# Optimization experiments

Hardware: AMD Instinct MI355X
Metric: run time of the kernel (lower is better)

Reference implementation:

```python
import jax, jax.numpy as jnp
import numpy as np

WS = (4, 4, 4)          # window size per axis
DISP = (2, 2, 2)        # cyclic-shift displacement = window_size // 2
HEADS = 8
HEAD_DIM = 32
DIM = 256


def _make_mask(x_shift, y_shift, z_shift):
    wx, wy, wz = WS
    dx, dy, dz = DISP
    m = np.zeros((wx, wy, wz, wx, wy, wz), np.float32)
    if x_shift:
        m[-dx:, :, :, :-dx, :, :] = -np.inf
        m[:-dx, :, :, -dx:, :, :] = -np.inf
    if y_shift:
        m[:, -dy:, :, :, :-dy, :] = -np.inf
        m[:, :-dy, :, :, -dy:, :] = -np.inf
    if z_shift:
        m[:, :, -dz:, :, :, :-dz] = -np.inf
        m[:, :, :-dz, :, :, -dz:] = -np.inf
    W = wx * wy * wz
    return jnp.asarray(m.reshape(W, W))


def setup_inputs() -> dict:
    key = jax.random.key(0)
    k1, k2, k3 = jax.random.split(key, 3)
    inner = HEADS * HEAD_DIM
    x = jax.random.normal(k1, (1, 48, 48, 48, DIM), jnp.float32)
    w_qkv = jax.random.normal(k2, (DIM, 3 * inner), jnp.float32) * (DIM ** -0.5)
    w_out = jax.random.normal(k3, (inner, DIM), jnp.float32) * (inner ** -0.5)
    b_out = jnp.zeros((DIM,), jnp.float32)
    return {"x": x, "w_qkv": w_qkv, "w_out": w_out, "b_out": b_out}


def reference(x, w_qkv, w_out, b_out):
    wx, wy, wz = WS
    h, d = HEADS, HEAD_DIM
    scale = d ** -0.5
    xm = _make_mask(True, False, False)
    ym = _make_mask(False, True, False)
    zm = _make_mask(False, False, True)

    # cyclic shift
    x = jnp.roll(x, (-DISP[0], -DISP[1], -DISP[2]), axis=(1, 2, 3))
    b, nx, ny, nz, _ = x.shape
    nwx, nwy, nwz = nx // wx, ny // wy, nz // wz
    W = wx * wy * wz
    nw = nwx * nwy * nwz

    qkv = x @ w_qkv                      # [b,nx,ny,nz,3*h*d]
    q, k, v = jnp.split(qkv, 3, axis=-1)

    def win(t):
        t = t.reshape(b, nwx, wx, nwy, wy, nwz, wz, h, d)
        t = t.transpose(0, 7, 1, 3, 5, 2, 4, 6, 8)   # b h nwx nwy nwz wx wy wz d
        return t.reshape(b, h, nw, W, d)

    q, k, v = win(q), win(k), win(v)
    dots = jnp.einsum('bhwid,bhwjd->bhwij', q, k) * scale

    # additive shift masks on the last window along each axis
    dots = dots.reshape(b, h, nwx, nwy, nwz, W, W)
    dots = dots.at[:, :, -1, :, :].add(xm)
    dots = dots.at[:, :, :, -1, :].add(ym)
    dots = dots.at[:, :, :, :, -1].add(zm)
    # faithful replication of original einops label mismatch: the tensor is
    # (nwx,nwy,nwz) but is flattened as if labeled (n_y,n_z,n_x) -> (n_x n_y n_z),
    # i.e. actual flatten order (nwz, nwx, nwy)
    dots = dots.transpose(0, 1, 4, 2, 3, 5, 6).reshape(b, h, nw, W, W)

    attn = jax.nn.softmax(dots, axis=-1)
    out = jnp.einsum('bhwij,bhwjd->bhwid', attn, v)

    out = out.reshape(b, h, nwx, nwy, nwz, wx, wy, wz, d)
    out = out.transpose(0, 2, 5, 3, 6, 4, 7, 1, 8).reshape(b, nx, ny, nz, h * d)
    out = out @ w_out + b_out
    # cyclic back shift
    return jnp.roll(out, DISP, axis=(1, 2, 3))
```

## Files before the change

kernel.cpp:

```cpp
#include <hip/hip_runtime.h>
#include <hip/hip_bf16.h>

typedef __attribute__((ext_vector_type(8))) short short8;
typedef __attribute__((ext_vector_type(4))) float f32x4;

#define NT 110592

static __device__ __forceinline__ unsigned int f2bf(float f){
  unsigned int x; __builtin_memcpy(&x,&f,4);
  x += 0x7fffu + ((x>>16)&1u);
  return x >> 16;
}

static __device__ __forceinline__ void gll16(const unsigned short* g, unsigned short* l){
  typedef const __attribute__((address_space(1))) unsigned int gu32;
  typedef __attribute__((address_space(3))) unsigned int lu32;
  __builtin_amdgcn_global_load_lds((gu32*)(const void*)g, (lu32*)(void*)l, 16, 0, 0);
}

__global__ void tpose(const float* __restrict__ in, unsigned short* __restrict__ out,
                      int R, int Cc){
  int id = blockIdx.x*256 + threadIdx.x;
  if (id < R*Cc){ int r = id / Cc, c = id - r*Cc; out[c*R + r] = (unsigned short)f2bf(in[id]); }
}

template<bool CF32, bool AF32>
__global__ __launch_bounds__(512, 8) void gemm_bt(
    const void* __restrict__ Av,
    const unsigned short* __restrict__ Bt,
    const float* __restrict__ bias,
    void* __restrict__ Cv,
    int M, int N, int K)
{
  __shared__ __align__(16) unsigned short As[2*4096];
  __shared__ __align__(16) unsigned short Bs[2*4096];

  const int nwg = gridDim.x;
  const int bid = blockIdx.x;
  const int qq = nwg >> 3, rr = nwg & 7;
  const int xcd = bid & 7, loc = bid >> 3;
  const int swz = (xcd < rr ? xcd*(qq+1) : rr*(qq+1) + (xcd-rr)*qq) + loc;
  const int nbn = N >> 7;
  const int bn = swz % nbn;
  const int bm = swz / nbn;

  const int tid  = threadIdx.x;
  const int lane = tid & 63;
  const int wave = tid >> 6;
  const int wm = wave >> 1, wn = wave & 1;
  const int l16 = lane & 15, q = lane >> 4;

  const int g8  = ((tid&3) ^ ((tid>>3)&3)) * 8;
  const int cg8 = (q ^ ((l16>>1)&3)) * 8;

  const size_t arow0 = (size_t)(bm*128 + (tid>>2))*K;
  const size_t brow0 = (size_t)(bn*128 + (tid>>2))*K;
  const unsigned short* Ab = (const unsigned short*)Av;
  const float*          Af = (const float*)Av;

  f32x4 acc[2][4] = {};

  for (int k0 = 0; k0 < K; k0 += 64){
    __syncthreads();
    if (AF32){
      const float* xa0 = Af + arow0 + k0 + g8;
      float4 a0 = *(const float4*)(xa0),      a1 = *(const float4*)(xa0+4);
      float4 b0 = *(const float4*)(xa0+32),   b1 = *(const float4*)(xa0+36);
      gll16(Bt + brow0 + k0 + g8,       &Bs[tid*8]);
      gll16(Bt + brow0 + k0 + 32 + g8,  &Bs[4096 + tid*8]);
      uint4 p0, p1;
      p0.x = f2bf(a0.x)|(f2bf(a0.y)<<16); p0.y = f2bf(a0.z)|(f2bf(a0.w)<<16);
      p0.z = f2bf(a1.x)|(f2bf(a1.y)<<16); p0.w = f2bf(a1.z)|(f2bf(a1.w)<<16);
      p1.x = f2bf(b0.x)|(f2bf(b0.y)<<16); p1.y = f2bf(b0.z)|(f2bf(b0.w)<<16);
      p1.z = f2bf(b1.x)|(f2bf(b1.y)<<16); p1.w = f2bf(b1.z)|(f2bf(b1.w)<<16);
      *(uint4*)&As[tid*8]        = p0;
      *(uint4*)&As[4096 + tid*8] = p1;
    } else {
      gll16(Ab + arow0 + k0 + g8,       &As[tid*8]);
      gll16(Ab + arow0 + k0 + 32 + g8,  &As[4096 + tid*8]);
      gll16(Bt + brow0 + k0 + g8,       &Bs[tid*8]);
      gll16(Bt + brow0 + k0 + 32 + g8,  &Bs[4096 + tid*8]);
    }
    __syncthreads();

    #pragma unroll
    for (int h = 0; h < 2; ++h){
      short8 af[2], bfm[4];
      #pragma unroll
      for (int t = 0; t < 2; ++t)
        af[t]  = *(const short8*)&As[h*4096 + (wm*32 + t*16 + l16)*32 + cg8];
      #pragma unroll
      for (int t = 0; t < 4; ++t)
        bfm[t] = *(const short8*)&Bs[h*4096 + (wn*64 + t*16 + l16)*32 + cg8];
      #pragma unroll
      for (int im = 0; im < 2; ++im)
        #pragma unroll
        for (int in = 0; in < 4; ++in)
          acc[im][in] = __builtin_amdgcn_mfma_f32_16x16x32_bf16(af[im], bfm[in], acc[im][in], 0, 0, 0);
    }
  }

  #pragma unroll
  for (int in = 0; in < 4; ++in){
    int col = bn*128 + wn*64 + in*16 + l16;
    float bv = CF32 ? bias[col] : 0.f;
    #pragma unroll
    for (int im = 0; im < 2; ++im){
      int row0 = bm*128 + wm*32 + im*16 + q*4;
      #pragma unroll
      for (int r = 0; r < 4; ++r){
        if (CF32) ((float*)Cv)[(size_t)(row0 + r)*N + col] = acc[im][in][r] + bv;
        else ((unsigned short*)Cv)[(size_t)(row0 + r)*N + col] = (unsigned short)f2bf(acc[im][in][r]);
      }
    }
  }
}

__global__ __launch_bounds__(256) void attn3d(
    const unsigned short* __restrict__ qkv,
    unsigned short* __restrict__ aout)
{
  __shared__ __align__(16) unsigned short sh[4*6912];
  const int tid  = threadIdx.x;
  const int wave = tid >> 6, lane = tid & 63;
  const int l16  = lane & 15, q = lane >> 4;
  unsigned short* P  = sh + wave*6912;
  unsigned short* VT = P + 64*72;

  const int wh   = blockIdx.x*4 + wave;
  const int head = wh & 7;
  const int w    = wh >> 3;
  const int A  = w / 144;
  const int B  = (w / 12) % 12;
  const int Cw = w % 12;

  const int iyy = l16 >> 2, izz = l16 & 3;
  int tok_qk[4], tok_v[4];
  #pragma unroll
  for (int t = 0; t < 4; ++t){
    int px = (4*B  + t   + 2) % 48;
    int py = (4*Cw + iyy + 2) % 48;
    int pz = (4*A  + izz + 2) % 48;
    tok_qk[t] = (px*48 + py)*48 + pz;
    int vx = (4*A  + t   + 2) % 48;
    int vy = (4*B  + iyy + 2) % 48;
    int vz = (4*Cw + izz + 2) % 48;
    tok_v[t] = (vx*48 + vy)*48 + vz;
  }

  {
    int sx = (4*A  + (lane>>4)     + 2) % 48;
    int sy = (4*B  + ((lane>>2)&3) + 2) % 48;
    int sz = (4*Cw + (lane&3)      + 2) % 48;
    const unsigned short* vp = qkv + (size_t)((sx*48+sy)*48+sz)*768 + 512 + head*32;
    uint4 v0 = *(const uint4*)(vp);
    uint4 v1 = *(const uint4*)(vp+8);
    uint4 v2 = *(const uint4*)(vp+16);
    uint4 v3 = *(const uint4*)(vp+24);
    unsigned vv[16] = {v0.x,v0.y,v0.z,v0.w, v1.x,v1.y,v1.z,v1.w,
                       v2.x,v2.y,v2.z,v2.w, v3.x,v3.y,v3.z,v3.w};
    #pragma unroll
    for (int u = 0; u < 16; ++u){
      VT[(2*u+0)*72 + lane] = (unsigned short)(vv[u] & 0xffffu);
      VT[(2*u+1)*72 + lane] = (unsigned short)(vv[u] >> 16);
    }
  }

  short8 kf[4], qf[4];
  #pragma unroll
  for (int t = 0; t < 4; ++t){
    const unsigned short* base = qkv + (size_t)tok_qk[t]*768 + head*32 + q*8;
    qf[t] = *(const short8*)(base);
    kf[t] = *(const short8*)(base + 256);
  }

  f32x4 s[4][4] = {};
  #pragma unroll
  for (int im = 0; im < 4; ++im)
    #pragma unroll
    for (int jn = 0; jn < 4; ++jn)
      s[im][jn] = __builtin_amdgcn_mfma_f32_16x16x32_bf16(kf[im], qf[jn], s[im][jn], 0, 0, 0);

  const float scale = 0.17677669529663687f;
  const int mx = (B == 11), my = (Cw == 11), mz = (A == 11);
  const int dy = my & ((q>>1) ^ (l16>>3));
  float sum4[4] = {0.f,0.f,0.f,0.f};
  #pragma unroll
  for (int jn = 0; jn < 4; ++jn){
    #pragma unroll
    for (int im = 0; im < 4; ++im){
      const int dxy = (mx & ((im>>1) ^ (jn>>1))) | dy;
      float e0 = (dxy | (mz & (0 ^ ((l16>>1)&1)))) ? 0.f : __expf(s[im][jn][0]*scale);
      float e1 = (dxy | (mz & (0 ^ ((l16>>1)&1)))) ? 0.f : __expf(s[im][jn][1]*scale);
      float e2 = (dxy | (mz & (1 ^ ((l16>>1)&1)))) ? 0.f : __expf(s[im][jn][2]*scale);
      float e3 = (dxy | (mz & (1 ^ ((l16>>1)&1)))) ? 0.f : __expf(s[im][jn][3]*scale);
      sum4[jn] += (e0+e1)+(e2+e3);
      uint2 pk;
      pk.x = f2bf(e0) | (f2bf(e1)<<16);
      pk.y = f2bf(e2) | (f2bf(e3)<<16);
      *(uint2*)&P[(jn*16+l16)*72 + im*16 + q*4] = pk;
    }
  }
  #pragma unroll
  for (int jn = 0; jn < 4; ++jn){
    float sj = sum4[jn];
    sj += __shfl_xor(sj, 16);
    sj += __shfl_xor(sj, 32);
    sum4[jn] = 1.f / sj;
  }

  f32x4 o[2][4] = {};
  #pragma unroll
  for (int ks = 0; ks < 2; ++ks){
    short8 vf[2], pf[4];
    #pragma unroll
    for (int dt = 0; dt < 2; ++dt)
      vf[dt] = *(const short8*)&VT[(dt*16 + l16)*72 + ks*32 + q*8];
    #pragma unroll
    for (int it = 0; it < 4; ++it)
      pf[it] = *(const short8*)&P[(it*16 + l16)*72 + ks*32 + q*8];
    #pragma unroll
    for (int dt = 0; dt < 2; ++dt)
      #pragma unroll
      for (int it = 0; it < 4; ++it)
        o[dt][it] = __builtin_amdgcn_mfma_f32_16x16x32_bf16(vf[dt], pf[it], o[dt][it], 0, 0, 0);
  }

  #pragma unroll
  for (int it = 0; it < 4; ++it){
    float inv = sum4[it];
    unsigned short* op = aout + (size_t)tok_v[it]*256 + head*32;
    #pragma unroll
    for (int dt = 0; dt < 2; ++dt){
      uint2 pk;
      pk.x = f2bf(o[dt][it][0]*inv) | (f2bf(o[dt][it][1]*inv) << 16);
      pk.y = f2bf(o[dt][it][2]*inv) | (f2bf(o[dt][it][3]*inv) << 16);
      *(uint2*)(op + dt*16 + q*4) = pk;
    }
  }
}

extern "C" void kernel_launch(void* const* d_in, const int* in_sizes, int n_in,
                              void* d_out, int out_size, void* d_ws, size_t ws_size,
                              hipStream_t stream) {
  const float* x     = (const float*)d_in[0];
  const float* w_qkv = (const float*)d_in[1];
  const float* w_out = (const float*)d_in[2];
  const float* b_out = (const float*)d_in[3];
  float* out = (float*)d_out;

  unsigned short* qkv   = (unsigned short*)d_ws;
  unsigned short* aout  = qkv   + (size_t)NT*768;
  unsigned short* wqkvT = aout  + (size_t)NT*256;
  unsigned short* woutT = wqkvT + (size_t)768*256;

  tpose<<<dim3((256*768 + 255)/256), dim3(256), 0, stream>>>(w_qkv, wqkvT, 256, 768);
  tpose<<<dim3((256*256 + 255)/256), dim3(256), 0, stream>>>(w_out, woutT, 256, 256);

  gemm_bt<false, true><<<dim3((768/128)*(NT/128)), dim3(512), 0, stream>>>(
      (const void*)x, wqkvT, nullptr, qkv, NT, 768, 256);

  attn3d<<<dim3(13824/4), dim3(256), 0, stream>>>(qkv, aout);

  gemm_bt<true, false><<<dim3((256/128)*(NT/128)), dim3(512), 0, stream>>>(
      (const void*)aout, woutT, b_out, out, NT, 256, 256);
}
```

Measured before the change: 377.0 us.

## Double-buffer GEMM LDS tiles to overlap next-slab loads with MFMA compute

Restructures the GEMM main loop from a single-buffered 64-wide K step into a 32-wide slab loop that ping-pongs between two LDS buffers. The loads for the next slab, including async global-to-LDS copies and the fp32 A loads, are issued before the MFMAs on the current slab, and the bf16 conversion store follows the compute. This cuts one barrier per iteration and hides global load latency behind compute. In exchange there are twice as many loop iterations, each with less MFMA work, and more registers are live.

New measurement: 805.4 us. 2.14x slower.

```diff
diff --git a/kernel.cpp b/kernel.cpp
--- a/kernel.cpp
+++ b/kernel.cpp
@@ -59,44 +59,58 @@
   const float*          Af = (const float*)Av;
 
   f32x4 acc[2][4] = {};
-
-  for (int k0 = 0; k0 < K; k0 += 64){
-    __syncthreads();
-    if (AF32){
-      const float* xa0 = Af + arow0 + k0 + g8;
-      float4 a0 = *(const float4*)(xa0),      a1 = *(const float4*)(xa0+4);
-      float4 b0 = *(const float4*)(xa0+32),   b1 = *(const float4*)(xa0+36);
-      gll16(Bt + brow0 + k0 + g8,       &Bs[tid*8]);
-      gll16(Bt + brow0 + k0 + 32 + g8,  &Bs[4096 + tid*8]);
-      uint4 p0, p1;
-      p0.x = f2bf(a0.x)|(f2bf(a0.y)<<16); p0.y = f2bf(a0.z)|(f2bf(a0.w)<<16);
-      p0.z = f2bf(a1.x)|(f2bf(a1.y)<<16); p0.w = f2bf(a1.z)|(f2bf(a1.w)<<16);
-      p1.x = f2bf(b0.x)|(f2bf(b0.y)<<16); p1.y = f2bf(b0.z)|(f2bf(b0.w)<<16);
-      p1.z = f2bf(b1.x)|(f2bf(b1.y)<<16); p1.w = f2bf(b1.z)|(f2bf(b1.w)<<16);
-      *(uint4*)&As[tid*8]        = p0;
-      *(uint4*)&As[4096 + tid*8] = p1;
-    } else {
-      gll16(Ab + arow0 + k0 + g8,       &As[tid*8]);
-      gll16(Ab + arow0 + k0 + 32 + g8,  &As[4096 + tid*8]);
-      gll16(Bt + brow0 + k0 + g8,       &Bs[tid*8]);
-      gll16(Bt + brow0 + k0 + 32 + g8,  &Bs[4096 + tid*8]);
-    }
-    __syncthreads();
-
-    #pragma unroll
-    for (int h = 0; h < 2; ++h){
-      short8 af[2], bfm[4];
+  const int nslab = K >> 5;
+
+  if (AF32){
+    gll16(Bt + brow0 + g8, &Bs[tid*8]);
+    const float* xa = Af + arow0 + g8;
+    float4 a0 = *(const float4*)xa, a1 = *(const float4*)(xa+4);
+    uint4 p;
+    p.x = f2bf(a0.x)|(f2bf(a0.y)<<16); p.y = f2bf(a0.z)|(f2bf(a0.w)<<16);
+    p.z = f2bf(a1.x)|(f2bf(a1.y)<<16); p.w = f2bf(a1.z)|(f2bf(a1.w)<<16);
+    *(uint4*)&As[tid*8] = p;
+  } else {
+    gll16(Ab + arow0 + g8, &As[tid*8]);
+    gll16(Bt + brow0 + g8, &Bs[tid*8]);
+  }
+  __syncthreads();
+
+  for (int t = 0; t < nslab; ++t){
+    const int cur = t & 1, nxt = cur ^ 1;
+
+    float4 a0, a1;
+    if (t + 1 < nslab){
+      const int k1 = (t+1) << 5;
+      if (AF32){
+        const float* xa = Af + arow0 + k1 + g8;
+        a0 = *(const float4*)xa; a1 = *(const float4*)(xa+4);
+      } else {
+        gll16(Ab + arow0 + k1 + g8, &As[nxt*4096 + tid*8]);
+      }
+      gll16(Bt + brow0 + k1 + g8, &Bs[nxt*4096 + tid*8]);
+    }
+
+    short8 af[2], bfm[4];
+    #pragma unroll
+    for (int tt = 0; tt < 2; ++tt)
+      af[tt]  = *(const short8*)&As[cur*4096 + (wm*32 + tt*16 + l16)*32 + cg8];
+    #pragma unroll
+    for (int tt = 0; tt < 4; ++tt)
+      bfm[tt] = *(const short8*)&Bs[cur*4096 + (wn*64 + tt*16 + l16)*32 + cg8];
+    #pragma unroll
+    for (int im = 0; im < 2; ++im)
       #pragma unroll
-      for (int t = 0; t < 2; ++t)
-        af[t]  = *(const short8*)&As[h*4096 + (wm*32 + t*16 + l16)*32 + cg8];
-      #pragma unroll
-      for (int t = 0; t < 4; ++t)
-        bfm[t] = *(const short8*)&Bs[h*4096 + (wn*64 + t*16 + l16)*32 + cg8];
-      #pragma unroll
-      for (int im = 0; im < 2; ++im)
-        #pragma unroll
-        for (int in = 0; in < 4; ++in)
-          acc[im][in] = __builtin_amdgcn_mfma_f32_16x16x32_bf16(af[im], bfm[in], acc[im][in], 0, 0, 0);
+      for (int in = 0; in < 4; ++in)
+        acc[im][in] = __builtin_amdgcn_mfma_f32_16x16x32_bf16(af[im], bfm[in], acc[im][in], 0, 0, 0);
+
+    if (t + 1 < nslab){
+      if (AF32){
+        uint4 p;
+        p.x = f2bf(a0.x)|(f2bf(a0.y)<<16); p.y = f2bf(a0.z)|(f2bf(a0.w)<<16);
+        p.z = f2bf(a1.x)|(f2bf(a1.y)<<16); p.w = f2bf(a1.z)|(f2bf(a1.w)<<16);
+        *(uint4*)&As[nxt*4096 + tid*8] = p;
+      }
+      __syncthreads();
     }
   }
 
```
